# Optimization experiments

Hardware: AMD Instinct MI355X
Metric: run time of the kernel (lower is better)

The kernel has to match this reference:

```python
import jax, jax.numpy as jnp
import numpy as np

N_NTYPES, N_ETYPES, H, D = 3, 5, 8, 32
N, E, C = 50000, 300000, 256


def setup_inputs() -> dict:
    key = jax.random.key(0)
    ks = jax.random.split(key, 13)
    s_c = 1.0 / np.sqrt(C)
    s_d = 1.0 / np.sqrt(D)
    return {
        "x": jax.random.normal(ks[0], (N, C), jnp.float32),
        "Wk": jax.random.normal(ks[1], (N_NTYPES, C, C), jnp.float32) * s_c,
        "Wq": jax.random.normal(ks[2], (N_NTYPES, C, C), jnp.float32) * s_c,
        "Wv": jax.random.normal(ks[3], (N_NTYPES, C, C), jnp.float32) * s_c,
        "Ratt": jax.random.normal(ks[4], (N_ETYPES, H, D, D), jnp.float32) * s_d,
        "Rmsg": jax.random.normal(ks[5], (N_ETYPES, H, D, D), jnp.float32) * s_d,
        "pri": jax.random.uniform(ks[6], (N_ETYPES, H), jnp.float32),
        "Wa": jax.random.normal(ks[7], (N_NTYPES, C, C), jnp.float32) * s_c,
        "skip": jax.random.normal(ks[8], (N_NTYPES,), jnp.float32),
        "src": jax.random.randint(ks[9], (E,), 0, N),
        "dst": jax.random.randint(ks[10], (E,), 0, N),
        "etype": jax.random.randint(ks[11], (E,), 0, N_ETYPES),
        "ntype": jax.random.randint(ks[12], (N,), 0, N_NTYPES),
    }


def typed_linear(x, W, types, n_types):
    # per-row weight selection by type; loop over small fixed #types
    out = jnp.zeros((x.shape[0], W.shape[-1]), x.dtype)
    for t in range(n_types):
        out = out + jnp.where((types == t)[:, None], x @ W[t], 0.0)
    return out


def reference(x, Wk, Wq, Wv, Ratt, Rmsg, pri, Wa, skip, src, dst, etype, ntype):
    n = x.shape[0]
    k = typed_linear(x, Wk, ntype, N_NTYPES).reshape(n, H, D)
    q = typed_linear(x, Wq, ntype, N_NTYPES).reshape(n, H, D)
    v = typed_linear(x, Wv, ntype, N_NTYPES).reshape(n, H, D)

    k_e = k[src]   # [E,H,D]
    v_e = v[src]   # [E,H,D]
    q_e = q[dst]   # [E,H,D]

    # per-edge-type, per-head DxD relation transforms (loop over small fixed #etypes)
    kw = jnp.zeros_like(k_e)
    mv = jnp.zeros_like(v_e)
    for r in range(N_ETYPES):
        m = (etype == r)[:, None, None]
        kw = kw + jnp.where(m, jnp.einsum('ehd,hdf->ehf', k_e, Ratt[r]), 0.0)
        mv = mv + jnp.where(m, jnp.einsum('ehd,hdf->ehf', v_e, Rmsg[r]), 0.0)

    # attention logits [E,H]
    a = (kw * q_e).sum(-1) * pri[etype] / jnp.sqrt(jnp.asarray(D, x.dtype))

    # edge softmax over incoming edges of each dst node, per head
    amax = jax.ops.segment_max(a, dst, num_segments=n)
    ex = jnp.exp(a - amax[dst])
    denom = jax.ops.segment_sum(ex, dst, num_segments=n)
    attn = ex / denom[dst]

    # weighted scatter-sum aggregation
    h = jax.ops.segment_sum(mv * attn[..., None], dst, num_segments=n)
    h = h.reshape(n, H * D)

    # typed output projection + sigmoid-gated skip (in_size == H*D)
    h = typed_linear(h, Wa, ntype, N_NTYPES)
    alpha = jax.nn.sigmoid(skip)[ntype][:, None]
    return h * alpha + x * (1.0 - alpha)
```

## Files before the change

### kernel.cpp

```cpp
#include <hip/hip_runtime.h>
#include <math.h>

#define CDIM 256
#define HD 8
#define DD 32
#define NT 3
#define ET 5
#define QWC (ET * CDIM)

typedef unsigned short u16;
typedef __attribute__((ext_vector_type(8))) short s16x8;
typedef __attribute__((ext_vector_type(4))) float f32x4;

__device__ __forceinline__ float b2f(u16 u) { return __uint_as_float(((unsigned)u) << 16); }
__device__ __forceinline__ u16 f2b(float x) {
    unsigned u = __float_as_uint(x);
    return (u16)((u + 0x7FFF + ((u >> 16) & 1)) >> 16);
}

__global__ void bhist_k(const int* __restrict__ ntype, int N, int nblk, int* __restrict__ bcnt) {
    __shared__ int wc[4][NT];
    int b = blockIdx.x, tid = threadIdx.x, lane = tid & 63, w = tid >> 6;
    int i = b * 256 + tid;
    int t = (i < N) ? ntype[i] : -1;
#pragma unroll
    for (int r = 0; r < NT; ++r) {
        unsigned long long m = __ballot(t == r);
        if (lane == 0) wc[w][r] = __popcll(m);
    }
    __syncthreads();
    if (tid < NT) bcnt[tid * nblk + b] = wc[0][tid] + wc[1][tid] + wc[2][tid] + wc[3][tid];
}

__global__ void bscan_k(const int* __restrict__ bcnt, int* __restrict__ base,
                        int* __restrict__ off, int total, int nblk, int N) {
    __shared__ int s[1024];
    int t = threadIdx.x;
    int v = (t < total) ? bcnt[t] : 0;
    s[t] = v; __syncthreads();
    for (int o = 1; o < 1024; o <<= 1) {
        int u = (t >= o) ? s[t - o] : 0; __syncthreads();
        s[t] += u; __syncthreads();
    }
    if (t < total) base[t] = s[t] - v;
    if (t < NT) off[t] = s[t * nblk] - bcnt[t * nblk];
    if (t == NT) off[NT] = N;
}

__global__ void bscatter_k(const int* __restrict__ ntype, int N, int nblk,
                           const int* __restrict__ base, int* __restrict__ perm) {
    __shared__ int wc[4][NT];
    __shared__ int woff[4][NT];
    int b = blockIdx.x, tid = threadIdx.x, lane = tid & 63, w = tid >> 6;
    int i = b * 256 + tid;
    int t = (i < N) ? ntype[i] : -1;
    unsigned long long mlt = (1ULL << lane) - 1;
    int rank = 0;
#pragma unroll
    for (int r = 0; r < NT; ++r) {
        unsigned long long m = __ballot(t == r);
        if (lane == 0) wc[w][r] = __popcll(m);
        if (t == r) rank = __popcll(m & mlt);
    }
    __syncthreads();
    if (tid == 0) {
#pragma unroll
        for (int r = 0; r < NT; ++r) {
            int a = 0;
#pragma unroll
            for (int w0 = 0; w0 < 4; ++w0) { woff[w0][r] = a; a += wc[w0][r]; }
        }
    }
    __syncthreads();
    if (t >= 0) perm[base[t * nblk + b] + woff[w][t] + rank] = i;
}

__global__ void ehist_k(const int* __restrict__ dst, const int* __restrict__ etype, int E,
                        int* __restrict__ khist) {
    int i = blockIdx.x * 256 + threadIdx.x;
    if (i < E) atomicAdd(&khist[dst[i] * ET + etype[i]], 1);
}

__global__ void kscan1_k(const int* __restrict__ khist, int* __restrict__ kscan,
                         int* __restrict__ bsum, int KEYS) {
    __shared__ int s[256];
    int b = blockIdx.x, t = threadIdx.x, i = b * 256 + t;
    int v = (i < KEYS) ? khist[i] : 0;
    s[t] = v; __syncthreads();
    for (int o = 1; o < 256; o <<= 1) {
        int u = (t >= o) ? s[t - o] : 0; __syncthreads();
        s[t] += u; __syncthreads();
    }
    if (i < KEYS) kscan[i] = s[t] - v;
    if (t == 255) bsum[b] = s[t];
}

__global__ void kscan2_k(int* __restrict__ bsum, int NB) {
    __shared__ int s[1024];
    int t = threadIdx.x;
    int v = (t < NB) ? bsum[t] : 0;
    s[t] = v; __syncthreads();
    for (int o = 1; o < 1024; o <<= 1) {
        int u = (t >= o) ? s[t - o] : 0; __syncthreads();
        s[t] += u; __syncthreads();
    }
    if (t < NB) bsum[t] = s[t] - v;
}

__global__ void kscan3r_k(int* __restrict__ kscan, const int* __restrict__ bsum,
                          int* __restrict__ rowptr, int KEYS, int E) {
    int i = blockIdx.x * 256 + threadIdx.x;
    if (i < KEYS) {
        int v = kscan[i] + bsum[blockIdx.x];
        kscan[i] = v;
        rowptr[i] = v;
    }
    if (i == 0) rowptr[KEYS] = E;
}

__global__ void escatter_k(const int* __restrict__ src, const int* __restrict__ dst,
                           const int* __restrict__ etype, int E,
                           int* __restrict__ kscan, int* __restrict__ epay) {
    int e = blockIdx.x * 256 + threadIdx.x;
    if (e < E) {
        int et = etype[e];
        int pos = atomicAdd(&kscan[dst[e] * ET + et], 1);
        epay[pos] = (et << 24) | src[e];
    }
}

__global__ __launch_bounds__(256) void wconv2_k(const float* __restrict__ Wk,
                                                const float* __restrict__ Wv,
                                                u16* __restrict__ Wtb) {
    __shared__ u16 s[64][72];
    int k0 = blockIdx.x * 64, c0 = blockIdx.y * 64, z = blockIdx.z;
    const float* Wp = (z < NT) ? (Wk + (size_t)z * CDIM * CDIM)
                               : (Wv + (size_t)(z - NT) * CDIM * CDIM);
    int r = threadIdx.x >> 2, q = (threadIdx.x & 3) * 16;
#pragma unroll
    for (int m = 0; m < 16; m += 4) {
        float4 v = *(const float4*)(Wp + (size_t)(k0 + r) * CDIM + c0 + q + m);
        s[r][q + m + 0] = f2b(v.x); s[r][q + m + 1] = f2b(v.y);
        s[r][q + m + 2] = f2b(v.z); s[r][q + m + 3] = f2b(v.w);
    }
    __syncthreads();
    int c = threadIdx.x >> 2, kq = (threadIdx.x & 3) * 16;
    u16* op = Wtb + ((size_t)z * CDIM + c0 + c) * CDIM + k0 + kq;
#pragma unroll
    for (int m = 0; m < 16; m += 4) {
        ushort4 o;
        o.x = s[kq + m + 0][c]; o.y = s[kq + m + 1][c];
        o.z = s[kq + m + 2][c]; o.w = s[kq + m + 3][c];
        *(ushort4*)(op + m) = o;
    }
}

__global__ __launch_bounds__(256) void rfold_k(const float* __restrict__ Wq,
                                               const float* __restrict__ Ratt,
                                               u16* __restrict__ qf_b,
                                               const float* __restrict__ Wa,
                                               const float* __restrict__ Rmsg,
                                               u16* __restrict__ af_b) {
    __shared__ float Rs[DD][DD];
    int b = blockIdx.x;
    int t = b / (ET * HD);
    int eh = b % (ET * HD);
    int et = eh >> 3, h = eh & 7;
    int tid = threadIdx.x;

    if (blockIdx.y == 0) {
        float4 rv = ((const float4*)(Ratt + (size_t)eh * (DD * DD)))[tid];
        int r = tid >> 3, c4 = (tid & 7) * 4;
        Rs[r][c4 + 0] = rv.x; Rs[r][c4 + 1] = rv.y;
        Rs[r][c4 + 2] = rv.z; Rs[r][c4 + 3] = rv.w;
        __syncthreads();

        int c = tid;
        const float* wr = Wq + (size_t)t * (CDIM * CDIM) + (size_t)c * CDIM + h * DD;
        float wrow[DD];
#pragma unroll
        for (int f = 0; f < DD; f += 4) {
            float4 v = *(const float4*)(wr + f);
            wrow[f] = v.x; wrow[f + 1] = v.y; wrow[f + 2] = v.z; wrow[f + 3] = v.w;
        }
        for (int m = 0; m < DD; ++m) {
            float acc = 0.f;
#pragma unroll
            for (int f = 0; f < DD; ++f) acc += wrow[f] * Rs[m][f];
            qf_b[((size_t)t * QWC + et * 256 + h * 32 + m) * CDIM + c] = f2b(acc);
        }
    } else {
        float4 rv = ((const float4*)(Rmsg + (size_t)eh * (DD * DD)))[tid];
        int r = tid >> 3, c4 = (tid & 7) * 4;
        Rs[r][c4 + 0] = rv.x; Rs[r][c4 + 1] = rv.y;
        Rs[r][c4 + 2] = rv.z; Rs[r][c4 + 3] = rv.w;
        __syncthreads();

        int col = tid;
        float wcol[DD];
#pragma unroll
        for (int m = 0; m < DD; ++m)
            wcol[m] = Wa[(size_t)t * (CDIM * CDIM) + (size_t)(h * 32 + m) * CDIM + col];

        u16* op = af_b + ((size_t)t * CDIM + col) * QWC + et * 256 + h * 32;
        for (int f = 0; f < DD; ++f) {
            float acc = 0.f;
#pragma unroll
            for (int m = 0; m < DD; ++m) acc += Rs[f][m] * wcol[m];
            op[f] = f2b(acc);
        }
    }
}

__global__ __launch_bounds__(256) void gemmall_k(
    const float* __restrict__ A, const u16* __restrict__ wtb, const u16* __restrict__ qf_b,
    u16* __restrict__ kb, u16* __restrict__ vb, u16* __restrict__ qwsv,
    const int* __restrict__ perm, const int* __restrict__ off, int N, int bpt)
{
    __shared__ u16 As[64][40];
    __shared__ u16 Bs[64][40];
    __shared__ int ridx[64];

    int t = blockIdx.y / bpt, bi = blockIdx.y % bpt;
    int i0 = off[t] + bi * 64, iend = off[t + 1];
    if (i0 >= iend) return;
    int tid = threadIdx.x;

    int bx = blockIdx.x;
    u16* out; int ostr, oc0; const u16* bslab;
    const size_t CC = (size_t)CDIM * CDIM;
    if (bx < 4)      { out = kb;   ostr = CDIM; oc0 = bx * 64;       bslab = wtb + (size_t)t * CC; }
    else if (bx < 8) { out = vb;   ostr = CDIM; oc0 = (bx - 4) * 64; bslab = wtb + (size_t)(NT + t) * CC; }
    else             { out = qwsv; ostr = QWC;  oc0 = (bx - 8) * 64; bslab = qf_b + (size_t)t * QWC * CDIM; }

    if (tid < 64) ridx[tid] = (i0 + tid < iend) ? perm[i0 + tid] : -1;
    __syncthreads();

    int sr = tid >> 2, sq = (tid & 3) * 8;
    int ar = ridx[sr];
    const float* asrc = A + (size_t)(ar < 0 ? 0 : ar) * CDIM + sq;
    const u16* bsrc = bslab + (size_t)(oc0 + sr) * CDIM + sq;

    auto loadA = [&](int k0) -> uint4 {
        uint4 r = make_uint4(0, 0, 0, 0);
        if (ar >= 0) {
            float4 a0 = *(const float4*)(asrc + k0);
            float4 a1 = *(const float4*)(asrc + k0 + 4);
            r.x = (unsigned)f2b(a0.x) | ((unsigned)f2b(a0.y) << 16);
            r.y = (unsigned)f2b(a0.z) | ((unsigned)f2b(a0.w) << 16);
            r.z = (unsigned)f2b(a1.x) | ((unsigned)f2b(a1.y) << 16);
            r.w = (unsigned)f2b(a1.z) | ((unsigned)f2b(a1.w) << 16);
        }
        return r;
    };

    int lane = tid & 63, wid = tid >> 6;
    int wr = wid >> 1, wc = wid & 1;
    int l15 = lane & 15, lk = (lane >> 4) * 8;

    f32x4 acc00 = {0.f, 0.f, 0.f, 0.f}, acc01 = {0.f, 0.f, 0.f, 0.f};
    f32x4 acc10 = {0.f, 0.f, 0.f, 0.f}, acc11 = {0.f, 0.f, 0.f, 0.f};

    uint4 apre = loadA(0);
    uint4 bpre = *(const uint4*)(bsrc);

    for (int k0 = 0; k0 < CDIM; k0 += 32) {
        __syncthreads();
        *(uint4*)&As[sr][sq] = apre;
        *(uint4*)&Bs[sr][sq] = bpre;
        __syncthreads();

        if (k0 + 32 < CDIM) {
            apre = loadA(k0 + 32);
            bpre = *(const uint4*)(bsrc + k0 + 32);
        }

        s16x8 af0 = *(const s16x8*)&As[wr * 32 + l15][lk];
        s16x8 af1 = *(const s16x8*)&As[wr * 32 + 16 + l15][lk];
        s16x8 bf0 = *(const s16x8*)&Bs[wc * 32 + l15][lk];
        s16x8 bf1 = *(const s16x8*)&Bs[wc * 32 + 16 + l15][lk];

        acc00 = __builtin_amdgcn_mfma_f32_16x16x32_bf16(af0, bf0, acc00, 0, 0, 0);
        acc01 = __builtin_amdgcn_mfma_f32_16x16x32_bf16(af0, bf1, acc01, 0, 0, 0);
        acc10 = __builtin_amdgcn_mfma_f32_16x16x32_bf16(af1, bf0, acc10, 0, 0, 0);
        acc11 = __builtin_amdgcn_mfma_f32_16x16x32_bf16(af1, bf1, acc11, 0, 0, 0);
    }

    int rbase = wr * 32 + (lane >> 4) * 4;
#pragma unroll
    for (int mi = 0; mi < 2; ++mi) {
#pragma unroll
        for (int r = 0; r < 4; ++r) {
            int lrow = rbase + mi * 16 + r;
            int node = ridx[lrow];
            if (node < 0) continue;
            float v0 = (mi == 0) ? acc00[r] : acc10[r];
            float v1 = (mi == 0) ? acc01[r] : acc11[r];
            size_t b0 = (size_t)node * ostr + oc0 + wc * 32 + l15;
            out[b0]      = f2b(v0);
            out[b0 + 16] = f2b(v1);
        }
    }
}

__global__ __launch_bounds__(256) void outgemm_k(
    const u16* __restrict__ svn, const u16* __restrict__ af_b, float* __restrict__ out,
    const int* __restrict__ perm, const int* __restrict__ off, int N, int bpt,
    const float* __restrict__ x, const float* __restrict__ skip)
{
    __shared__ u16 As[64][68];
    __shared__ int ridx[64];

    int t = blockIdx.x / bpt, bi = blockIdx.x % bpt;
    int i0 = off[t] + bi * 64, iend = off[t + 1];
    if (i0 >= iend) return;
    int tid = threadIdx.x;
    if (tid < 64) ridx[tid] = (i0 + tid < iend) ? perm[i0 + tid] : -1;
    __syncthreads();

    int lane = tid & 63, y = tid >> 6;
    int l15 = lane & 15, lq = lane >> 4;
    int lk = lq * 8;

    int sr = tid >> 2, sc = (tid & 3) * 16;
    int ar = ridx[sr];
    const u16* asrc = svn + (size_t)(ar < 0 ? 0 : ar) * QWC + sc;
    const u16* bbase = af_b + ((size_t)t * CDIM + y * 64) * QWC;

    f32x4 acc[4][4];
#pragma unroll
    for (int mi = 0; mi < 4; ++mi)
#pragma unroll
        for (int ci = 0; ci < 4; ++ci)
            acc[mi][ci] = (f32x4){0.f, 0.f, 0.f, 0.f};

    uint4 apre0 = make_uint4(0, 0, 0, 0), apre1 = make_uint4(0, 0, 0, 0);
    if (ar >= 0) {
        apre0 = *(const uint4*)(asrc);
        apre1 = *(const uint4*)(asrc + 8);
    }

    for (int kc = 0; kc < 20; ++kc) {
        __syncthreads();
        *(uint4*)&As[sr][sc] = apre0;
        *(uint4*)&As[sr][sc + 8] = apre1;
        __syncthreads();
        if (kc + 1 < 20) {
            int ko = (kc + 1) * 64;
            if (ar >= 0) {
                apre0 = *(const uint4*)(asrc + ko);
                apre1 = *(const uint4*)(asrc + ko + 8);
            }
        }

        int kbase = kc * 64;
        s16x8 bf0[4], bf1[4];
#pragma unroll
        for (int ci = 0; ci < 4; ++ci) {
            const u16* bp = bbase + (size_t)(ci * 16 + l15) * QWC + kbase;
            bf0[ci] = *(const s16x8*)(bp + lk);
            bf1[ci] = *(const s16x8*)(bp + 32 + lk);
        }

#pragma unroll
        for (int mi = 0; mi < 4; ++mi) {
            s16x8 af0 = *(const s16x8*)&As[mi * 16 + l15][lk];
            s16x8 af1 = *(const s16x8*)&As[mi * 16 + l15][32 + lk];
#pragma unroll
            for (int ci = 0; ci < 4; ++ci) {
                acc[mi][ci] = __builtin_amdgcn_mfma_f32_16x16x32_bf16(af0, bf0[ci], acc[mi][ci], 0, 0, 0);
                acc[mi][ci] = __builtin_amdgcn_mfma_f32_16x16x32_bf16(af1, bf1[ci], acc[mi][ci], 0, 0, 0);
            }
        }
    }

    float alpha = 1.f / (1.f + __expf(-skip[t]));
    float beta = 1.f - alpha;
#pragma unroll
    for (int mi = 0; mi < 4; ++mi) {
#pragma unroll
        for (int r = 0; r < 4; ++r) {
            int node = ridx[mi * 16 + lq * 4 + r];
            if (node < 0) continue;
#pragma unroll
            for (int ci = 0; ci < 4; ++ci) {
                size_t b0 = (size_t)node * CDIM + y * 64 + ci * 16 + l15;
                out[b0] = acc[mi][ci][r] * alpha + x[b0] * beta;
            }
        }
    }
}

__global__ __launch_bounds__(256) void gather3_k(
    const u16* __restrict__ kb, const u16* __restrict__ vb, u16* __restrict__ qwsv,
    const float* __restrict__ pri, const int* __restrict__ rowptr, const int* __restrict__ epay,
    int N)
{
    int d = (blockIdx.x * 256 + threadIdx.x) >> 6;
    if (d >= N) return;
    int lane = threadIdx.x & 63, h = lane >> 3;
    const float rsD = 0.17677669529663687f;
    size_t rowb = (size_t)d * QWC + lane * 4;

    ushort4 qu0 = *(const ushort4*)(qwsv + rowb);
    ushort4 qu1 = *(const ushort4*)(qwsv + rowb + 256);
    ushort4 qu2 = *(const ushort4*)(qwsv + rowb + 512);
    ushort4 qu3 = *(const ushort4*)(qwsv + rowb + 768);
    ushort4 qu4 = *(const ushort4*)(qwsv + rowb + 1024);

    int p0 = __builtin_amdgcn_readfirstlane(rowptr[d * ET]);
    int p1 = __builtin_amdgcn_readfirstlane(rowptr[d * ET + ET]);

    float Sv0[4] = {0,0,0,0}, Sv1[4] = {0,0,0,0}, Sv2[4] = {0,0,0,0};
    float Sv3[4] = {0,0,0,0}, Sv4[4] = {0,0,0,0};
    float a0 = 0.f, a1 = 0.f, a2 = 0.f, a3 = 0.f, dsum = 0.f;
    int cur_et = -1;
    float cq0 = 0.f, cq1 = 0.f, cq2 = 0.f, cq3 = 0.f, cpf = 0.f;

    int payc = 0; ushort4 kuc = {0,0,0,0}, vuc = {0,0,0,0};
    if (p0 < p1) {
        payc = epay[p0];
        int s = payc & 0xFFFFFF;
        kuc = *(const ushort4*)(kb + (size_t)s * CDIM + lane * 4);
        vuc = *(const ushort4*)(vb + (size_t)s * CDIM + lane * 4);
    }

    for (int p = p0; p < p1; ++p) {
        int payn = 0; ushort4 kun = {0,0,0,0}, vun = {0,0,0,0};
        if (p + 1 < p1) {
            payn = epay[p + 1];
            int sn = payn & 0xFFFFFF;
            kun = *(const ushort4*)(kb + (size_t)sn * CDIM + lane * 4);
            vun = *(const ushort4*)(vb + (size_t)sn * CDIM + lane * 4);
        }
        int et = __builtin_amdgcn_readfirstlane(payc) >> 24;
        if (et != cur_et) {
            switch (cur_et) {
                case 0: Sv0[0]=a0; Sv0[1]=a1; Sv0[2]=a2; Sv0[3]=a3; break;
                case 1: Sv1[0]=a0; Sv1[1]=a1; Sv1[2]=a2; Sv1[3]=a3; break;
                case 2: Sv2[0]=a0; Sv2[1]=a1; Sv2[2]=a2; Sv2[3]=a3; break;
                case 3: Sv3[0]=a0; Sv3[1]=a1; Sv3[2]=a2; Sv3[3]=a3; break;
                default: break;
            }
            a0 = a1 = a2 = a3 = 0.f;
            cur_et = et;
            ushort4 q = (et == 0) ? qu0 : (et == 1) ? qu1 : (et == 2) ? qu2
                       : (et == 3) ? qu3 : qu4;
            cq0 = b2f(q.x); cq1 = b2f(q.y); cq2 = b2f(q.z); cq3 = b2f(q.w);
            cpf = pri[et * HD + h] * rsD;
        }
        float t = b2f(kuc.x) * cq0 + b2f(kuc.y) * cq1 + b2f(kuc.z) * cq2 + b2f(kuc.w) * cq3;
        t += __shfl_xor(t, 1, 8);
        t += __shfl_xor(t, 2, 8);
        t += __shfl_xor(t, 4, 8);
        float ex = __expf(t * cpf);
        a0 += ex * b2f(vuc.x); a1 += ex * b2f(vuc.y);
        a2 += ex * b2f(vuc.z); a3 += ex * b2f(vuc.w);
        dsum += ex;
        payc = payn; kuc = kun; vuc = vun;
    }
    switch (cur_et) {
        case 0: Sv0[0]=a0; Sv0[1]=a1; Sv0[2]=a2; Sv0[3]=a3; break;
        case 1: Sv1[0]=a0; Sv1[1]=a1; Sv1[2]=a2; Sv1[3]=a3; break;
        case 2: Sv2[0]=a0; Sv2[1]=a1; Sv2[2]=a2; Sv2[3]=a3; break;
        case 3: Sv3[0]=a0; Sv3[1]=a1; Sv3[2]=a2; Sv3[3]=a3; break;
        case 4: Sv4[0]=a0; Sv4[1]=a1; Sv4[2]=a2; Sv4[3]=a3; break;
        default: break;
    }

    float inv = dsum > 0.f ? 1.f / dsum : 0.f;
    ushort4 o;
    o.x=f2b(Sv0[0]*inv); o.y=f2b(Sv0[1]*inv); o.z=f2b(Sv0[2]*inv); o.w=f2b(Sv0[3]*inv);
    *(ushort4*)(qwsv + rowb) = o;
    o.x=f2b(Sv1[0]*inv); o.y=f2b(Sv1[1]*inv); o.z=f2b(Sv1[2]*inv); o.w=f2b(Sv1[3]*inv);
    *(ushort4*)(qwsv + rowb + 256) = o;
    o.x=f2b(Sv2[0]*inv); o.y=f2b(Sv2[1]*inv); o.z=f2b(Sv2[2]*inv); o.w=f2b(Sv2[3]*inv);
    *(ushort4*)(qwsv + rowb + 512) = o;
    o.x=f2b(Sv3[0]*inv); o.y=f2b(Sv3[1]*inv); o.z=f2b(Sv3[2]*inv); o.w=f2b(Sv3[3]*inv);
    *(ushort4*)(qwsv + rowb + 768) = o;
    o.x=f2b(Sv4[0]*inv); o.y=f2b(Sv4[1]*inv); o.z=f2b(Sv4[2]*inv); o.w=f2b(Sv4[3]*inv);
    *(ushort4*)(qwsv + rowb + 1024) = o;
}

extern "C" void kernel_launch(void* const* d_in, const int* in_sizes, int n_in,
                              void* d_out, int out_size, void* d_ws, size_t ws_size,
                              hipStream_t stream) {
    const float* x    = (const float*)d_in[0];
    const float* Wk   = (const float*)d_in[1];
    const float* Wq   = (const float*)d_in[2];
    const float* Wv   = (const float*)d_in[3];
    const float* Ratt = (const float*)d_in[4];
    const float* Rmsg = (const float*)d_in[5];
    const float* pri  = (const float*)d_in[6];
    const float* Wa   = (const float*)d_in[7];
    const float* skip = (const float*)d_in[8];
    const int* src   = (const int*)d_in[9];
    const int* dst   = (const int*)d_in[10];
    const int* etype = (const int*)d_in[11];
    const int* ntype = (const int*)d_in[12];

    int N = in_sizes[12];
    int E = in_sizes[9];
    const size_t NC = (size_t)N * CDIM;
    const int KEYS = N * ET;
    const int NB = (KEYS + 255) / 256;
    const int nblk = (N + 255) / 256;
    const size_t WTE = (size_t)NT * CDIM * CDIM;
    const size_t QFE = (size_t)NT * QWC * CDIM;

    u16* kb   = (u16*)d_ws;
    u16* vb   = kb + NC;
    u16* qwsv = vb + NC;
    u16* wtb  = qwsv + 5 * NC;
    u16* qf_b = wtb + 2 * WTE;
    u16* af_b = qf_b + QFE;
    int* rowptr = (int*)(af_b + QFE);
    int* perm   = rowptr + KEYS + 1;
    int* epay   = perm + N;
    int* off    = epay + E;
    int* khist = (int*)qwsv;
    int* kscan = khist + KEYS;
    int* bsum  = kscan + KEYS;
    int* bcnt  = bsum + 1024;
    int* base  = bcnt + NT * nblk;

    hipMemsetAsync(khist, 0, (size_t)KEYS * sizeof(int), stream);

    bhist_k<<<nblk, 256, 0, stream>>>(ntype, N, nblk, bcnt);
    bscan_k<<<1, 1024, 0, stream>>>(bcnt, base, off, NT * nblk, nblk, N);
    bscatter_k<<<nblk, 256, 0, stream>>>(ntype, N, nblk, base, perm);

    ehist_k<<<(E + 255) / 256, 256, 0, stream>>>(dst, etype, E, khist);
    kscan1_k<<<NB, 256, 0, stream>>>(khist, kscan, bsum, KEYS);
    kscan2_k<<<1, 1024, 0, stream>>>(bsum, NB);
    kscan3r_k<<<NB, 256, 0, stream>>>(kscan, bsum, rowptr, KEYS, E);
    escatter_k<<<(E + 255) / 256, 256, 0, stream>>>(src, dst, etype, E, kscan, epay);

    wconv2_k<<<dim3(4, 4, 2 * NT), 256, 0, stream>>>(Wk, Wv, wtb);
    rfold_k<<<dim3(NT * ET * HD, 2), 256, 0, stream>>>(Wq, Ratt, qf_b, Wa, Rmsg, af_b);

    int bpt = (N + 63) / 64;

    gemmall_k<<<dim3(28, NT * bpt), 256, 0, stream>>>(x, wtb, qf_b, kb, vb, qwsv,
                                                      perm, off, N, bpt);

    gather3_k<<<(N * 64 + 255) / 256, 256, 0, stream>>>(kb, vb, qwsv, pri, rowptr, epay, N);

    outgemm_k<<<NT * bpt, 256, 0, stream>>>(qwsv, af_b, (float*)d_out, perm, off, N, bpt,
                                            x, skip);
}
```

Baseline: 428.8 us.

## Pre-convert x to bf16 and remap gemm blocks so XCDs share A panels

Adds a pass that converts x to bf16 once into the output buffer as scratch, so the fused K/V/Q gemm reads half the A bytes and skips repeated per-block fp32-to-bf16 conversion across its 28 column blocks. The gemm grid becomes 1D, with block ids mapped so that all 28 column tiles of a row panel land on the same XCD (bid&7), improving L2 reuse of the A panel. The cost is an extra kernel launch and a full read/write of x, plus padded no-op blocks.

```diff
diff --git a/kernel.cpp b/kernel.cpp
--- a/kernel.cpp
+++ b/kernel.cpp
@@ -127,6 +127,14 @@
         int pos = atomicAdd(&kscan[dst[e] * ET + et], 1);
         epay[pos] = (et << 24) | src[e];
     }
+}
+
+__global__ void f2bv_k(const float* __restrict__ in, u16* __restrict__ out, size_t n4) {
+    size_t i = (size_t)blockIdx.x * 256 + threadIdx.x;
+    if (i >= n4) return;
+    float4 v = ((const float4*)in)[i];
+    ushort4 o; o.x = f2b(v.x); o.y = f2b(v.y); o.z = f2b(v.z); o.w = f2b(v.w);
+    ((ushort4*)out)[i] = o;
 }
 
 __global__ __launch_bounds__(256) void wconv2_k(const float* __restrict__ Wk,
@@ -213,20 +221,26 @@
 }
 
 __global__ __launch_bounds__(256) void gemmall_k(
-    const float* __restrict__ A, const u16* __restrict__ wtb, const u16* __restrict__ qf_b,
+    const u16* __restrict__ xb, const u16* __restrict__ wtb, const u16* __restrict__ qf_b,
     u16* __restrict__ kb, u16* __restrict__ vb, u16* __restrict__ qwsv,
-    const int* __restrict__ perm, const int* __restrict__ off, int N, int bpt)
+    const int* __restrict__ perm, const int* __restrict__ off, int N, int bpt, int npanel)
 {
     __shared__ u16 As[64][40];
     __shared__ u16 Bs[64][40];
     __shared__ int ridx[64];
 
-    int t = blockIdx.y / bpt, bi = blockIdx.y % bpt;
+    int bid = blockIdx.x;
+    int xcd = bid & 7;
+    int rr_ = bid >> 3;
+    int g = rr_ / 28, bx = rr_ % 28;
+    int p = g * 8 + xcd;
+    if (p >= npanel) return;
+    int t = p / bpt, bi = p % bpt;
+
     int i0 = off[t] + bi * 64, iend = off[t + 1];
     if (i0 >= iend) return;
     int tid = threadIdx.x;
 
-    int bx = blockIdx.x;
     u16* out; int ostr, oc0; const u16* bslab;
     const size_t CC = (size_t)CDIM * CDIM;
     if (bx < 4)      { out = kb;   ostr = CDIM; oc0 = bx * 64;       bslab = wtb + (size_t)t * CC; }
@@ -238,21 +252,8 @@
 
     int sr = tid >> 2, sq = (tid & 3) * 8;
     int ar = ridx[sr];
-    const float* asrc = A + (size_t)(ar < 0 ? 0 : ar) * CDIM + sq;
+    const u16* asrc = xb + (size_t)(ar < 0 ? 0 : ar) * CDIM + sq;
     const u16* bsrc = bslab + (size_t)(oc0 + sr) * CDIM + sq;
-
-    auto loadA = [&](int k0) -> uint4 {
-        uint4 r = make_uint4(0, 0, 0, 0);
-        if (ar >= 0) {
-            float4 a0 = *(const float4*)(asrc + k0);
-            float4 a1 = *(const float4*)(asrc + k0 + 4);
-            r.x = (unsigned)f2b(a0.x) | ((unsigned)f2b(a0.y) << 16);
-            r.y = (unsigned)f2b(a0.z) | ((unsigned)f2b(a0.w) << 16);
-            r.z = (unsigned)f2b(a1.x) | ((unsigned)f2b(a1.y) << 16);
-            r.w = (unsigned)f2b(a1.z) | ((unsigned)f2b(a1.w) << 16);
-        }
-        return r;
-    };
 
     int lane = tid & 63, wid = tid >> 6;
     int wr = wid >> 1, wc = wid & 1;
@@ -261,7 +262,8 @@
     f32x4 acc00 = {0.f, 0.f, 0.f, 0.f}, acc01 = {0.f, 0.f, 0.f, 0.f};
     f32x4 acc10 = {0.f, 0.f, 0.f, 0.f}, acc11 = {0.f, 0.f, 0.f, 0.f};
 
-    uint4 apre = loadA(0);
+    uint4 apre = make_uint4(0, 0, 0, 0);
+    if (ar >= 0) apre = *(const uint4*)(asrc);
     uint4 bpre = *(const uint4*)(bsrc);
 
     for (int k0 = 0; k0 < CDIM; k0 += 32) {
@@ -271,7 +273,7 @@
         __syncthreads();
 
         if (k0 + 32 < CDIM) {
-            apre = loadA(k0 + 32);
+            if (ar >= 0) apre = *(const uint4*)(asrc + k0 + 32);
             bpre = *(const uint4*)(bsrc + k0 + 32);
         }
 
@@ -524,6 +526,8 @@
     int* bcnt  = bsum + 1024;
     int* base  = bcnt + NT * nblk;
 
+    u16* xb = (u16*)d_out;
+
     hipMemsetAsync(khist, 0, (size_t)KEYS * sizeof(int), stream);
 
     bhist_k<<<nblk, 256, 0, stream>>>(ntype, N, nblk, bcnt);
@@ -538,11 +542,15 @@
 
     wconv2_k<<<dim3(4, 4, 2 * NT), 256, 0, stream>>>(Wk, Wv, wtb);
     rfold_k<<<dim3(NT * ET * HD, 2), 256, 0, stream>>>(Wq, Ratt, qf_b, Wa, Rmsg, af_b);
+    size_t n4 = NC / 4;
+    f2bv_k<<<(int)((n4 + 255) / 256), 256, 0, stream>>>(x, xb, n4);
 
     int bpt = (N + 63) / 64;
-
-    gemmall_k<<<dim3(28, NT * bpt), 256, 0, stream>>>(x, wtb, qf_b, kb, vb, qwsv,
-                                                      perm, off, N, bpt);
+    int npanel = NT * bpt;
+    int ppad = (npanel + 7) & ~7;
+
+    gemmall_k<<<ppad * 28, 256, 0, stream>>>(xb, wtb, qf_b, kb, vb, qwsv,
+                                             perm, off, N, bpt, npanel);
 
     gather3_k<<<(N * 64 + 255) / 256, 256, 0, stream>>>(kb, vb, qwsv, pri, rowptr, epay, N);
 
```

Measured after the change: 419.1 us. 2.3% less time.
